# Performance work log

Hardware: AMD Instinct MI355X
Metric: run time of the kernel (lower is better)

Reference implementation:

```python
import jax, jax.numpy as jnp
import numpy as np

D_MODEL = 64
N_HEAD = 4
HEAD_DIM = D_MODEL // N_HEAD  # 16


def setup_inputs() -> dict:
    key = jax.random.key(0)
    ks = jax.random.split(key, 8)
    B, T_dec, T_enc = 16, 1024, 1024
    s = 1.0 / np.sqrt(D_MODEL)
    return {
        "x": jax.random.normal(ks[0], (B, T_dec, D_MODEL), dtype=jnp.float32),
        "encoder_outputs": jax.random.normal(ks[1], (B, T_enc, D_MODEL), dtype=jnp.float32),
        "encoder_outputs_mask": jnp.ones((B, T_enc), dtype=jnp.int32),
        "Wkv": jax.random.normal(ks[2], (D_MODEL, 2 * D_MODEL), dtype=jnp.float32) * s,
        "bkv": jnp.zeros((2 * D_MODEL,), dtype=jnp.float32),
        "Wq": jax.random.normal(ks[3], (D_MODEL, D_MODEL), dtype=jnp.float32) * s,
        "bq": jnp.zeros((D_MODEL,), dtype=jnp.float32),
        "Wproj": jax.random.normal(ks[4], (D_MODEL, D_MODEL), dtype=jnp.float32) * s,
        "bproj": jnp.zeros((D_MODEL,), dtype=jnp.float32),
    }


def reference(x, encoder_outputs, encoder_outputs_mask, Wkv, bkv, Wq, bq, Wproj, bproj):
    B, T_dec, C = x.shape
    T_enc = encoder_outputs.shape[1]
    kv = encoder_outputs @ Wkv + bkv                      # [B, T_enc, 2C]
    k, v = kv[..., :D_MODEL], kv[..., D_MODEL:]          # [B, T_enc, C]
    q = x @ Wq + bq                                      # [B, T_dec, C]
    q = q.reshape(B, T_dec, N_HEAD, HEAD_DIM)
    k = k.reshape(B, T_enc, N_HEAD, HEAD_DIM)
    v = v.reshape(B, T_enc, N_HEAD, HEAD_DIM)
    scale = 1.0 / jnp.sqrt(jnp.asarray(HEAD_DIM, dtype=q.dtype))
    att = jnp.einsum("bqhd,bkhd->bhqk", q, k) * scale    # [B, H, T_dec, T_enc]
    mask = (encoder_outputs_mask == 0)[:, None, None, :]  # [B, 1, 1, T_enc]
    att = jnp.where(mask, jnp.asarray(-jnp.inf, dtype=att.dtype), att)
    att = jax.nn.softmax(att, axis=-1)
    ctx = jnp.einsum("bhqk,bkhd->bqhd", att, v).reshape(B, T_dec, C)
    # dropout is identity at eval time
    return ctx @ Wproj + bproj
```

## Files before the change

kernel.cpp:

```cpp
#include <hip/hip_runtime.h>
#include <hip/hip_bf16.h>
#include <math.h>

#define DM 64
#define NH 4
#define HD 16
#define BATCH 16
#define TSEQ 1024

typedef short bf16x8 __attribute__((ext_vector_type(8)));
typedef short bf16x4 __attribute__((ext_vector_type(4)));
typedef float f32x4  __attribute__((ext_vector_type(4)));
typedef float f32x16 __attribute__((ext_vector_type(16)));

static __device__ inline short f2bf(float x) {
    __hip_bfloat16 h = __float2bfloat16(x);
    return __builtin_bit_cast(short, h);
}
static __device__ inline float bf2f(short s) {
    __hip_bfloat16 h = __builtin_bit_cast(__hip_bfloat16, s);
    return __bfloat162float(h);
}

__global__ __launch_bounds__(256) void proj_kernel(
    const float* __restrict__ x, const float* __restrict__ enc,
    const float* __restrict__ Wkv, const float* __restrict__ bkv,
    const float* __restrict__ Wq,  const float* __restrict__ bq,
    const int* __restrict__ mask,
    short* __restrict__ qhi, short* __restrict__ qlo,
    short* __restrict__ khi, short* __restrict__ klo,
    short* __restrict__ vtt)
{
    const int t = threadIdx.x;
    const int part = blockIdx.y;
    const int r = blockIdx.x * 256 + t;
    const int b = r >> 10, trow = r & 1023;

    const float* in; const float* W; const float* bias; int cb, ldw;
    if (part < 4)      { in = x;   W = Wq;  ldw = 64;  cb = part*16;          bias = bq;  }
    else if (part < 8) { in = enc; W = Wkv; ldw = 128; cb = (part-4)*16;      bias = bkv; }
    else               { in = enc; W = Wkv; ldw = 128; cb = 64 + (part-8)*16; bias = bkv; }

    __shared__ float wsl[64][16];
    for (int idx = t; idx < 1024; idx += 256)
        wsl[idx >> 4][idx & 15] = W[(idx >> 4)*ldw + cb + (idx & 15)];

    float4 xr[16];
    const float4* inrow = (const float4*)(in + (size_t)r * 64);
    #pragma unroll
    for (int i = 0; i < 16; ++i) xr[i] = inrow[i];
    __syncthreads();

    float acc[16];
    #pragma unroll
    for (int j = 0; j < 16; ++j) acc[j] = bias[cb + j];
    #pragma unroll
    for (int k = 0; k < 64; ++k) {
        const float xv = ((const float*)xr)[k];
        const float4 w0 = ((const float4*)&wsl[k][0])[0];
        const float4 w1 = ((const float4*)&wsl[k][0])[1];
        const float4 w2 = ((const float4*)&wsl[k][0])[2];
        const float4 w3 = ((const float4*)&wsl[k][0])[3];
        acc[0]  += xv*w0.x; acc[1]  += xv*w0.y; acc[2]  += xv*w0.z; acc[3]  += xv*w0.w;
        acc[4]  += xv*w1.x; acc[5]  += xv*w1.y; acc[6]  += xv*w1.z; acc[7]  += xv*w1.w;
        acc[8]  += xv*w2.x; acc[9]  += xv*w2.y; acc[10] += xv*w2.z; acc[11] += xv*w2.w;
        acc[12] += xv*w3.x; acc[13] += xv*w3.y; acc[14] += xv*w3.z; acc[15] += xv*w3.w;
    }

    if (part < 8) {
        const float scale = (part < 4) ? 0.36067376022224085f : 1.0f;
        short* dh = (part < 4) ? qhi : khi;
        short* dl = (part < 4) ? qlo : klo;
        const int h = (part < 4) ? part : (part - 4);
        bf16x8 h0, h1, l0, l1;
        #pragma unroll
        for (int j = 0; j < 16; ++j) {
            float vf = acc[j] * scale;
            short hb = f2bf(vf);
            short lb = f2bf(vf - bf2f(hb));
            if (j < 8) { h0[j] = hb; l0[j] = lb; }
            else       { h1[j-8] = hb; l1[j-8] = lb; }
        }
        size_t off = (((size_t)(b*NH + h))*TSEQ + trow)*HD;
        *(bf16x8*)(dh + off)     = h0;
        *(bf16x8*)(dh + off + 8) = h1;
        *(bf16x8*)(dl + off)     = l0;
        *(bf16x8*)(dl + off + 8) = l1;
    } else {
        const int h = part - 8;
        const float mb = (mask[b*TSEQ + trow] != 0) ? 1.0f : 0.0f;
        short* tile = vtt + ((size_t)(b*NH + h))*32768 + (size_t)(trow >> 5)*1024;
        const int kw = trow & 31;
        #pragma unroll
        for (int j = 0; j < 16; ++j)
            tile[j*32 + kw] = f2bf(acc[j] * mb);
        tile[16*32 + kw] = (mb != 0.0f) ? (short)0x3F80 : (short)0;
    }
}

__global__ __launch_bounds__(512) void attn_kernel(
    const short* __restrict__ qhi, const short* __restrict__ qlo,
    const short* __restrict__ khi, const short* __restrict__ klo,
    const short* __restrict__ vtt,
    const float* __restrict__ Wproj, const float* __restrict__ bproj,
    float* __restrict__ out)
{
    const int tid  = threadIdx.x;
    const int lane = tid & 63;
    const int wid  = __builtin_amdgcn_readfirstlane(tid >> 6);
    const int h  = wid & 3;
    const int ks = wid >> 2;
    const int qbase = blockIdx.x * 32;
    const int b  = blockIdx.y;
    const int l31 = lane & 31, half = lane >> 5;

    __shared__ short Pb[8][32][36];
    __shared__ float Cbuf[2][32][67];
    __shared__ float Lbuf[2][NH][32];

    const size_t qoff = (((size_t)(b*NH + h))*TSEQ + qbase + l31)*HD + half*8;
    const bf16x8 qAh = *(const bf16x8*)(qhi + qoff);
    const bf16x8 qAl = *(const bf16x8*)(qlo + qoff);

    const short* khb = khi + (((size_t)(b*NH + h))*TSEQ + ks*512)*HD;
    const short* klb = klo + (((size_t)(b*NH + h))*TSEQ + ks*512)*HD;
    const short* vtb = vtt + ((size_t)(b*NH + h))*32768 + (size_t)ks*16384;

    f32x16 Cacc;
    #pragma unroll
    for (int i = 0; i < 16; ++i) Cacc[i] = 0.f;

    short* pw = &Pb[wid][0][0];
    const short* pr = &Pb[wid][l31][0];

    for (int step = 0; step < 16; ++step) {
        const int ko = step * 32;
        const bf16x8 kBh = *(const bf16x8*)(khb + (size_t)(ko + l31)*HD + half*8);
        const bf16x8 kBl = *(const bf16x8*)(klb + (size_t)(ko + l31)*HD + half*8);
        const short* tile = vtb + (size_t)step * 1024;
        const bf16x8 vB0 = *(const bf16x8*)(tile + l31*32 + half*8);
        const bf16x8 vB1 = *(const bf16x8*)(tile + l31*32 + 16 + half*8);

        f32x16 S;
        #pragma unroll
        for (int i = 0; i < 16; ++i) S[i] = 0.f;
        S = __builtin_amdgcn_mfma_f32_32x32x16_bf16(qAh, kBh, S, 0, 0, 0);
        S = __builtin_amdgcn_mfma_f32_32x32x16_bf16(qAh, kBl, S, 0, 0, 0);
        S = __builtin_amdgcn_mfma_f32_32x32x16_bf16(qAl, kBh, S, 0, 0, 0);

        #pragma unroll
        for (int i = 0; i < 16; ++i) {
            const float p = __builtin_amdgcn_exp2f(S[i]);
            const int row = (i & 3) + 8*(i >> 2) + 4*half;
            pw[row*36 + l31] = f2bf(p);
        }

        const bf16x4 a0 = *(const bf16x4*)(pr + half*8);
        const bf16x4 a1 = *(const bf16x4*)(pr + half*8 + 4);
        const bf16x4 a2 = *(const bf16x4*)(pr + 16 + half*8);
        const bf16x4 a3 = *(const bf16x4*)(pr + 16 + half*8 + 4);
        const bf16x8 pA0 = __builtin_shufflevector(a0, a1, 0, 1, 2, 3, 4, 5, 6, 7);
        const bf16x8 pA1 = __builtin_shufflevector(a2, a3, 0, 1, 2, 3, 4, 5, 6, 7);

        Cacc = __builtin_amdgcn_mfma_f32_32x32x16_bf16(pA0, vB0, Cacc, 0, 0, 0);
        Cacc = __builtin_amdgcn_mfma_f32_32x32x16_bf16(pA1, vB1, Cacc, 0, 0, 0);
    }

    #pragma unroll
    for (int r = 0; r < 16; ++r) {
        const int row = (r & 3) + 8*(r >> 2) + 4*half;
        if (l31 < 16)        Cbuf[ks][row][h*HD + l31] = Cacc[r];
        else if (l31 == 16)  Lbuf[ks][h][row] = Cacc[r];
    }
    __syncthreads();

    const int q   = tid >> 4;
    const int cbo = (tid & 15) * 4;
    float linv[NH];
    #pragma unroll
    for (int hh = 0; hh < NH; ++hh)
        linv[hh] = 1.0f / (Lbuf[0][hh][q] + Lbuf[1][hh][q]);

    float o0 = bproj[cbo], o1 = bproj[cbo+1], o2 = bproj[cbo+2], o3 = bproj[cbo+3];
    #pragma unroll
    for (int i = 0; i < 64; ++i) {
        const float cv = (Cbuf[0][q][i] + Cbuf[1][q][i]) * linv[i >> 4];
        const float4 wr = *(const float4*)(Wproj + i*DM + cbo);
        o0 += cv*wr.x; o1 += cv*wr.y; o2 += cv*wr.z; o3 += cv*wr.w;
    }
    float4 st; st.x = o0; st.y = o1; st.z = o2; st.w = o3;
    *(float4*)(out + ((size_t)b*TSEQ + qbase + q)*DM + cbo) = st;
}

extern "C" void kernel_launch(void* const* d_in, const int* in_sizes, int n_in,
                              void* d_out, int out_size, void* d_ws, size_t ws_size,
                              hipStream_t stream) {
    const float* x     = (const float*)d_in[0];
    const float* enc   = (const float*)d_in[1];
    const int*   mask  = (const int*)  d_in[2];
    const float* Wkv   = (const float*)d_in[3];
    const float* bkv   = (const float*)d_in[4];
    const float* Wq    = (const float*)d_in[5];
    const float* bq    = (const float*)d_in[6];
    const float* Wproj = (const float*)d_in[7];
    const float* bproj = (const float*)d_in[8];
    float* out = (float*)d_out;

    const size_t SZ = (size_t)BATCH*NH*TSEQ*HD;
    short* qhi = (short*)d_ws;
    short* qlo = qhi + SZ;
    short* khi = qlo + SZ;
    short* klo = khi + SZ;
    short* vtt = klo + SZ;

    proj_kernel<<<dim3(64, 12), dim3(256), 0, stream>>>(
        x, enc, Wkv, bkv, Wq, bq, mask, qhi, qlo, khi, klo, vtt);
    attn_kernel<<<dim3(32, 16), dim3(512), 0, stream>>>(
        qhi, qlo, khi, klo, vtt, Wproj, bproj, out);
}
```

Baseline: 110.8 us.

## Keep softmax probabilities in registers via transposed QK MFMA and permlane swaps

Result: no change. 110.0 us (-0.8%).

```diff
diff --git a/kernel.cpp b/kernel.cpp
--- a/kernel.cpp
+++ b/kernel.cpp
@@ -12,6 +12,7 @@
 typedef short bf16x4 __attribute__((ext_vector_type(4)));
 typedef float f32x4  __attribute__((ext_vector_type(4)));
 typedef float f32x16 __attribute__((ext_vector_type(16)));
+typedef unsigned int u32x4 __attribute__((ext_vector_type(4)));
 
 static __device__ inline short f2bf(float x) {
     __hip_bfloat16 h = __float2bfloat16(x);
@@ -20,6 +21,11 @@
 static __device__ inline float bf2f(short s) {
     __hip_bfloat16 h = __builtin_bit_cast(__hip_bfloat16, s);
     return __bfloat162float(h);
+}
+static __device__ inline unsigned pkbf(float a, float b) {
+    unsigned r;
+    asm("v_cvt_pk_bf16_f32 %0, %1, %2" : "=v"(r) : "v"(a), "v"(b));
+    return r;
 }
 
 __global__ __launch_bounds__(256) void proj_kernel(
@@ -114,7 +120,6 @@
     const int b  = blockIdx.y;
     const int l31 = lane & 31, half = lane >> 5;
 
-    __shared__ short Pb[8][32][36];
     __shared__ float Cbuf[2][32][67];
     __shared__ float Lbuf[2][NH][32];
 
@@ -129,9 +134,6 @@
     f32x16 Cacc;
     #pragma unroll
     for (int i = 0; i < 16; ++i) Cacc[i] = 0.f;
-
-    short* pw = &Pb[wid][0][0];
-    const short* pr = &Pb[wid][l31][0];
 
     for (int step = 0; step < 16; ++step) {
         const int ko = step * 32;
@@ -144,23 +146,26 @@
         f32x16 S;
         #pragma unroll
         for (int i = 0; i < 16; ++i) S[i] = 0.f;
-        S = __builtin_amdgcn_mfma_f32_32x32x16_bf16(qAh, kBh, S, 0, 0, 0);
-        S = __builtin_amdgcn_mfma_f32_32x32x16_bf16(qAh, kBl, S, 0, 0, 0);
-        S = __builtin_amdgcn_mfma_f32_32x32x16_bf16(qAl, kBh, S, 0, 0, 0);
-
-        #pragma unroll
-        for (int i = 0; i < 16; ++i) {
-            const float p = __builtin_amdgcn_exp2f(S[i]);
-            const int row = (i & 3) + 8*(i >> 2) + 4*half;
-            pw[row*36 + l31] = f2bf(p);
-        }
-
-        const bf16x4 a0 = *(const bf16x4*)(pr + half*8);
-        const bf16x4 a1 = *(const bf16x4*)(pr + half*8 + 4);
-        const bf16x4 a2 = *(const bf16x4*)(pr + 16 + half*8);
-        const bf16x4 a3 = *(const bf16x4*)(pr + 16 + half*8 + 4);
-        const bf16x8 pA0 = __builtin_shufflevector(a0, a1, 0, 1, 2, 3, 4, 5, 6, 7);
-        const bf16x8 pA1 = __builtin_shufflevector(a2, a3, 0, 1, 2, 3, 4, 5, 6, 7);
+        S = __builtin_amdgcn_mfma_f32_32x32x16_bf16(kBh, qAh, S, 0, 0, 0);
+        S = __builtin_amdgcn_mfma_f32_32x32x16_bf16(kBl, qAh, S, 0, 0, 0);
+        S = __builtin_amdgcn_mfma_f32_32x32x16_bf16(kBh, qAl, S, 0, 0, 0);
+
+        float p[16];
+        #pragma unroll
+        for (int i = 0; i < 16; ++i) p[i] = __builtin_amdgcn_exp2f(S[i]);
+
+        unsigned a0 = pkbf(p[0],  p[1]),  b0 = pkbf(p[4],  p[5]);
+        unsigned a1 = pkbf(p[2],  p[3]),  b1 = pkbf(p[6],  p[7]);
+        unsigned a2 = pkbf(p[8],  p[9]),  b2 = pkbf(p[12], p[13]);
+        unsigned a3 = pkbf(p[10], p[11]), b3 = pkbf(p[14], p[15]);
+        asm("v_permlane32_swap_b32 %0, %1" : "+v"(a0), "+v"(b0));
+        asm("v_permlane32_swap_b32 %0, %1" : "+v"(a1), "+v"(b1));
+        asm("v_permlane32_swap_b32 %0, %1" : "+v"(a2), "+v"(b2));
+        asm("v_permlane32_swap_b32 %0, %1" : "+v"(a3), "+v"(b3));
+        u32x4 P0v; P0v[0] = a0; P0v[1] = a1; P0v[2] = b0; P0v[3] = b1;
+        u32x4 P1v; P1v[0] = a2; P1v[1] = a3; P1v[2] = b2; P1v[3] = b3;
+        const bf16x8 pA0 = __builtin_bit_cast(bf16x8, P0v);
+        const bf16x8 pA1 = __builtin_bit_cast(bf16x8, P1v);
 
         Cacc = __builtin_amdgcn_mfma_f32_32x32x16_bf16(pA0, vB0, Cacc, 0, 0, 0);
         Cacc = __builtin_amdgcn_mfma_f32_32x32x16_bf16(pA1, vB1, Cacc, 0, 0, 0);
```
